# Performance work log

Hardware: AMD Instinct MI355X
Metric: run time of the kernel (lower is better)

## Reference

```python
import jax, jax.numpy as jnp
import numpy as np

NUM_EMBEDDINGS = 16384
EMBEDDING_DIM = 256
B, C, H, W = 8, 256, 32, 32


def _l2_normalize(x, axis=-1, eps=1e-12):
    # matches torch.nn.functional.normalize(p=2): x / max(||x||, eps)
    n = jnp.sqrt(jnp.sum(x * x, axis=axis, keepdims=True))
    return x / jnp.maximum(n, eps)


def setup_inputs() -> dict:
    key = jax.random.key(0)
    k1, k2 = jax.random.split(key)
    z = jax.random.normal(k1, (B, C, H, W), dtype=jnp.float32)
    embedding_weight = jax.random.normal(k2, (NUM_EMBEDDINGS, EMBEDDING_DIM), dtype=jnp.float32)
    return {"z": z, "embedding_weight": embedding_weight}


def reference(z, embedding_weight):
    batch_size, channels, height, width = z.shape
    # [B,C,H,W] -> [B,H,W,C] -> [N, D]
    z_flat = jnp.transpose(z, (0, 2, 3, 1)).reshape(-1, EMBEDDING_DIM)
    z_flat = _l2_normalize(z_flat)                 # l2_norm=True
    emb = _l2_normalize(embedding_weight)
    # squared distances: ||z||^2 + ||e||^2 - 2 z e^T  -> [N, K]
    d = (jnp.sum(z_flat * z_flat, axis=1, keepdims=True)
         + jnp.sum(emb * emb, axis=1)
         - 2.0 * jnp.matmul(z_flat, emb.T))
    indices = jnp.argmin(d, axis=1)                # [N]
    z_q = emb[indices].reshape(batch_size, height, width, EMBEDDING_DIM)
    z_q = jnp.transpose(z_q, (0, 3, 1, 2))         # [B,C,H,W]
    indices = indices.reshape(batch_size, height, width)
    return z_q, indices
```

## Files before the change

kernel.cpp:

```cpp
#include <hip/hip_runtime.h>

#define NUM_E   16384
#define DIM     256
#define NROWS   8192
#define HW      1024
#define BM      128
#define BN      128
#define BK      32
#define NCB     (NUM_E / BN)
#define GATE    2.5e-3f
#define TAUC    2.5e-3f
#define EHID    2.5e-3
#define MAXC    16

#define SWZ(r) ((((r) >> 1) ^ ((r) >> 3)) & 3)

typedef __bf16 bf16x8 __attribute__((ext_vector_type(8)));
typedef float  f32x4  __attribute__((ext_vector_type(4)));
typedef float  f32x16 __attribute__((ext_vector_type(16)));

__device__ __forceinline__ unsigned short f2bf(float x) {
    unsigned u = __float_as_uint(x);
    unsigned r = (u + 0x7fffu + ((u >> 16) & 1u)) >> 16;
    return (unsigned short)r;
}
__device__ __forceinline__ void async_copy16(const void* g, void* l) {
    __builtin_amdgcn_global_load_lds(
        (const __attribute__((address_space(1))) unsigned int*)g,
        (__attribute__((address_space(3))) unsigned int*)l, 16, 0, 0);
}
__device__ __forceinline__ int imax(int a, int b) { return a > b ? a : b; }
__device__ __forceinline__ int imin(int a, int b) { return a < b ? a : b; }

__global__ void k_prep_z(const float* __restrict__ z, unsigned short* __restrict__ Zh) {
    __shared__ float T[64 * 68];
    __shared__ float P[16][68];
    __shared__ __align__(16) float Tinv[64];
    int t = threadIdx.x;
    int n0 = blockIdx.x * 64;
    int b = n0 >> 10, hw0 = n0 & 1023;
    {
        int cg = t >> 4, h4 = (t & 15) * 4;
        float4 s4 = make_float4(0.f, 0.f, 0.f, 0.f);
        const float* pz = z + (size_t)(b * DIM + cg * 16) * HW + hw0 + h4;
        #pragma unroll
        for (int cc = 0; cc < 16; cc++) {
            float4 v = *(const float4*)(pz + (size_t)cc * HW);
            s4.x += v.x * v.x; s4.y += v.y * v.y; s4.z += v.z * v.z; s4.w += v.w * v.w;
        }
        *(float4*)&P[cg][h4] = s4;
    }
    __syncthreads();
    if (t < 64) {
        float s = 0.f;
        #pragma unroll
        for (int cg = 0; cg < 16; cg++) s += P[cg][t];
        Tinv[t] = 1.0f / fmaxf(sqrtf(s), 1e-12f);
    }
    __syncthreads();
    for (int c0 = 0; c0 < DIM; c0 += 64) {
        #pragma unroll
        for (int i = 0; i < 4; i++) {
            int f = t + 256 * i;
            int cc = f >> 4, n4 = (f & 15) * 4;
            float4 v  = *(const float4*)(z + (size_t)(b * DIM + c0 + cc) * HW + hw0 + n4);
            float4 iv = *(const float4*)&Tinv[n4];
            v.x *= iv.x; v.y *= iv.y; v.z *= iv.z; v.w *= iv.w;
            *(float4*)&T[cc * 68 + n4] = v;
        }
        __syncthreads();
        #pragma unroll
        for (int i = 0; i < 4; i++) {
            int f = t + 256 * i;
            int nn = f >> 4, c4 = (f & 15) * 4;
            ushort4 h;
            h.x = f2bf(T[(c4+0)*68 + nn]);
            h.y = f2bf(T[(c4+1)*68 + nn]);
            h.z = f2bf(T[(c4+2)*68 + nn]);
            h.w = f2bf(T[(c4+3)*68 + nn]);
            *(ushort4*)(Zh + (size_t)(n0 + nn) * DIM + c0 + c4) = h;
        }
        __syncthreads();
    }
}

__global__ void k_prep_e(const float* __restrict__ emb, float* __restrict__ inv_e,
                         double* __restrict__ se2, unsigned short* __restrict__ Eh,
                         int* __restrict__ cnt, int* __restrict__ cnt2) {
    if (blockIdx.x == 0 && threadIdx.x == 0) { *cnt = 0; *cnt2 = 0; }
    int wv = threadIdx.x >> 6, lane = threadIdx.x & 63;
    int k = blockIdx.x * 4 + wv;
    float4 v = *(const float4*)(emb + (size_t)k * DIM + lane * 4);
    double sq = (double)v.x*v.x + (double)v.y*v.y + (double)v.z*v.z + (double)v.w*v.w;
    for (int off = 32; off > 0; off >>= 1) sq += __shfl_down(sq, off);
    double tot = fmax(__shfl(sq, 0), 1e-24);
    if (lane == 0) { se2[k] = tot; inv_e[k] = 1.0f / fmaxf((float)sqrt(tot), 1e-12f); }
    float s = 1.0f / fmaxf((float)sqrt(tot), 1e-12f);
    ushort4 h;
    h.x = f2bf(v.x * s); h.y = f2bf(v.y * s); h.z = f2bf(v.z * s); h.w = f2bf(v.w * s);
    *(ushort4*)(Eh + (size_t)k * DIM + lane * 4) = h;
}

__launch_bounds__(256, 3)
__global__ void k_score(const unsigned short* __restrict__ Zh,
                        const unsigned short* __restrict__ Eh, int2* __restrict__ part) {
    __shared__ __align__(16) int smem[12288];
    unsigned short* lds = (unsigned short*)smem;
    int* kv = smem;
    const int t = threadIdx.x, l = t & 63, w = t >> 6;
    const int wm = w >> 1, wn = w & 1;
    const int m0 = blockIdx.x * BM;
    const int nb = blockIdx.y * BN;
    const int l31 = l & 31, lh = l >> 5;
    const int sr = l >> 2, sp = l & 3;

    const unsigned short* gA0 = Zh + (size_t)m0 * DIM;
    const unsigned short* gB0 = Eh + (size_t)nb * DIM;

    f32x16 acc[2][2];
    #pragma unroll
    for (int i = 0; i < 2; i++)
        #pragma unroll
        for (int j = 0; j < 2; j++) acc[i][j] = (f32x16)2.0f;

    auto stage = [&](int dbase, int kc) {
        #pragma unroll
        for (int h = 0; h < 2; h++) {
            int sub = w * 2 + h;
            int r = sub * 16 + sr;
            int c = sp ^ SWZ(r);
            async_copy16(gA0 + (size_t)r * DIM + kc + c * 8, &lds[dbase + sub * 512]);
        }
        #pragma unroll
        for (int h = 0; h < 2; h++) {
            int sub = w * 2 + h;
            int r = sub * 16 + sr;
            int c = sp ^ SWZ(r);
            async_copy16(gB0 + (size_t)r * DIM + kc + c * 8, &lds[dbase + 4096 + sub * 512]);
        }
    };

    stage(0, 0);
    stage(8192, BK);
    for (int kt = 0; kt < DIM / BK; kt++) {
        const int base = (kt % 3) * 8192;
        if (kt < DIM / BK - 1) asm volatile("s_waitcnt vmcnt(4)" ::: "memory");
        else                   asm volatile("s_waitcnt vmcnt(0)" ::: "memory");
        __builtin_amdgcn_s_barrier();
        asm volatile("" ::: "memory");
        bf16x8 ah[2][2], bh[2][2];
        #pragma unroll
        for (int s = 0; s < 2; s++) {
            int c = 2 * s + lh;
            #pragma unroll
            for (int i = 0; i < 2; i++) {
                int r = wm * 64 + i * 32 + l31;
                ah[s][i] = *(const bf16x8*)&lds[base + r * 32 + ((c ^ SWZ(r)) * 8)];
            }
            #pragma unroll
            for (int j = 0; j < 2; j++) {
                int r = wn * 64 + j * 32 + l31;
                bh[s][j] = *(const bf16x8*)&lds[base + 4096 + r * 32 + ((c ^ SWZ(r)) * 8)];
            }
        }
        if (kt + 2 < DIM / BK) stage(((kt + 2) % 3) * 8192, (kt + 2) * BK);
        __builtin_amdgcn_s_setprio(1);
        #pragma unroll
        for (int s = 0; s < 2; s++)
            #pragma unroll
            for (int i = 0; i < 2; i++)
                #pragma unroll
                for (int j = 0; j < 2; j++)
                    acc[i][j] = __builtin_amdgcn_mfma_f32_32x32x16_bf16(ah[s][i], bh[s][j], acc[i][j], 0, 0, 0);
        __builtin_amdgcn_s_setprio(0);
    }
    __syncthreads();

    const int cb0 = wn * 64 + l31;
    int KA1 = 0, KA2 = 0, KB1 = 0, KB2 = 0;
    const int rl = t >> 2, q = t & 3;
    #pragma unroll
    for (int i = 0; i < 2; i++) {
        #pragma unroll
        for (int reg = 0; reg < 16; reg++) {
            int k0 = (__float_as_int(acc[i][0][reg]) & 0xFFFFFF00) | cb0;
            int k1 = (__float_as_int(acc[i][1][reg]) & 0xFFFFFF00) | (cb0 + 32);
            int K1 = imax(k0, k1), K2 = imin(k0, k1);
            int rr = wm * 32 + (reg & 3) + 8 * (reg >> 2) + 4 * lh;
            int slot = wn * 32 + l31;
            *(int2*)&kv[(rr * 66 + slot) * 2] = make_int2(K1, K2);
        }
        __syncthreads();
        int S1 = 0, S2 = 0;
        const int2* pr = (const int2*)&kv[(rl * 66 + q * 16) * 2];
        #pragma unroll
        for (int u = 0; u < 16; u++) {
            int2 e = pr[u];
            S2 = imax(imax(S2, e.y), imin(S1, e.x));
            S1 = imax(S1, e.x);
        }
        __syncthreads();
        #pragma unroll
        for (int d2 = 1; d2 <= 2; d2 <<= 1) {
            int o1 = __shfl_down(S1, d2), o2 = __shfl_down(S2, d2);
            S2 = imax(imax(S2, o2), imin(S1, o1));
            S1 = imax(S1, o1);
        }
        if (i == 0) { KA1 = S1; KA2 = S2; } else { KB1 = S1; KB2 = S2; }
    }
    if ((t & 3) == 0) {
        int rowA = (rl >> 5) * 64 + (rl & 31);
        int rowB = rowA + 32;
        part[(size_t)blockIdx.y * NROWS + m0 + rowA] = make_int2(KA1, KA2);
        part[(size_t)blockIdx.y * NROWS + m0 + rowB] = make_int2(KB1, KB2);
    }
}

__global__ void k_final(const int2* __restrict__ part, int* __restrict__ idx_ws,
                        float* __restrict__ out_idx, int* __restrict__ flags,
                        int* __restrict__ cnt, int* __restrict__ cand,
                        int* __restrict__ ccnt, float* __restrict__ v2q) {
    __shared__ int rK1[8][33], rK2[8][33], rS[8][33];
    __shared__ int bK1[32], bK2[32];
    __shared__ int lcc[32];
    __shared__ int lcand[32][MAXC];
    __shared__ int sv2[8][33];
    const int nl = threadIdx.x & 31, sc = threadIdx.x >> 5;
    const int n = blockIdx.x * 32 + nl;
    if (threadIdx.x < 32) lcc[threadIdx.x] = 0;
    int K1 = 0, K2 = 0, S1 = 0;
    for (int s = sc * 16; s < sc * 16 + 16; s++) {
        int2 e = part[(size_t)s * NROWS + n];
        S1 = (e.x > K1) ? s : S1;
        int nK2 = imax(imin(K1, e.x), imax(K2, e.y));
        K1 = imax(K1, e.x);
        K2 = nK2;
    }
    rK1[sc][nl] = K1; rK2[sc][nl] = K2; rS[sc][nl] = S1;
    __syncthreads();
    if (threadIdx.x < 32) {
        int W1 = 0, W2 = 0, WS = 0;
        #pragma unroll
        for (int s2 = 0; s2 < 8; s2++) {
            int e1 = rK1[s2][threadIdx.x], e2 = rK2[s2][threadIdx.x];
            WS = (e1 > W1) ? rS[s2][threadIdx.x] : WS;
            int nW2 = imax(imin(W1, e1), imax(W2, e2));
            W1 = imax(W1, e1);
            W2 = nW2;
        }
        int nn = blockIdx.x * 32 + threadIdx.x;
        int J1 = WS * BN + (W1 & 0xFF);
        idx_ws[nn] = J1;
        out_idx[nn] = (float)J1;
        bK1[threadIdx.x] = W1;
        bK2[threadIdx.x] = W2;
    }
    __syncthreads();
    int kthr = __float_as_int(__int_as_float(bK1[nl] & 0xFFFFFF00) - TAUC);
    int lv2 = 0;
    for (int s = sc * 16; s < sc * 16 + 16; s++) {
        int2 e = part[(size_t)s * NROWS + n];
        if (e.x >= kthr) {
            int pos = atomicAdd(&lcc[nl], 2);
            if (pos < MAXC)     lcand[nl][pos]     = s * BN + (e.x & 0xFF);
            if (pos + 1 < MAXC) lcand[nl][pos + 1] = s * BN + (e.y & 0xFF);
            lv2 = imax(lv2, e.y);
        }
    }
    sv2[sc][nl] = lv2;
    __syncthreads();
    if (threadIdx.x < 32) {
        int nn = blockIdx.x * 32 + threadIdx.x;
        float v1 = __int_as_float(bK1[threadIdx.x] & 0xFFFFFF00) - 2.0f;
        float v2 = __int_as_float(bK2[threadIdx.x] & 0xFFFFFF00) - 2.0f;
        if (v1 - v2 < GATE) {
            int m = 0;
            #pragma unroll
            for (int s2 = 0; s2 < 8; s2++) m = imax(m, sv2[s2][threadIdx.x]);
            int p = atomicAdd(cnt, 1);
            flags[p] = nn;
            ccnt[nn] = lcc[threadIdx.x];
            v2q[nn] = __int_as_float(m & 0xFFFFFF00) - 2.0f;
            #pragma unroll
            for (int j = 0; j < MAXC; j++) cand[nn * MAXC + j] = lcand[threadIdx.x][j];
        }
    }
}

__launch_bounds__(256)
__global__ void k_rescan_cand(const int* __restrict__ flags, const int* __restrict__ cnt,
                              const int* __restrict__ cand, const int* __restrict__ ccnt,
                              const float* __restrict__ v2q,
                              const float* __restrict__ z, const float* __restrict__ emb,
                              const double* __restrict__ se2,
                              int* __restrict__ idx_ws, float* __restrict__ out_idx,
                              int* __restrict__ flags2, int* __restrict__ cnt2) {
    __shared__ double zs[DIM];
    __shared__ double wv[4];
    __shared__ int    wi[4];
    const int t = threadIdx.x, l = t & 63, w = t >> 6;
    const int F = *cnt;
    for (int f = blockIdx.x; f < F; f += gridDim.x) {
        int n = flags[f];
        int C = ccnt[n];
        int b = n >> 10, hw = n & 1023;
        __syncthreads();
        zs[t] = (double)z[(size_t)(b * DIM + t) * HW + hw];
        __syncthreads();
        double best = -2e18; int bi = 0x7fffffff;
        if (C <= MAXC) {
            double z0 = zs[l*4], z1 = zs[l*4+1], z2 = zs[l*4+2], z3 = zs[l*4+3];
            for (int cix = w; cix < C; cix += 4) {
                int k = cand[n * MAXC + cix];
                float4 ev = *(const float4*)(emb + (size_t)k * DIM + l * 4);
                double d = z0 * (double)ev.x + z1 * (double)ev.y
                         + z2 * (double)ev.z + z3 * (double)ev.w;
                #pragma unroll
                for (int o = 32; o > 0; o >>= 1) d += __shfl_down(d, o);
                if (l == 0) {
                    double qv = d / sqrt(se2[k]);
                    if (qv > best || (qv == best && k < bi)) { best = qv; bi = k; }
                }
            }
        }
        if (l == 0) { wv[w] = best; wi[w] = bi; }
        __syncthreads();
        if (t == 0) {
            if (C > MAXC) {
                int p = atomicAdd(cnt2, 1); flags2[p] = n;
            } else {
                double B = wv[0]; int BI = wi[0];
                #pragma unroll
                for (int x = 1; x < 4; x++)
                    if (wv[x] > B || (wv[x] == B && wi[x] < BI)) { B = wv[x]; BI = wi[x]; }
                if ((double)v2q[n] >= B - EHID) {
                    int p = atomicAdd(cnt2, 1); flags2[p] = n;
                } else {
                    idx_ws[n] = BI; out_idx[n] = (float)BI;
                }
            }
        }
    }
}

__launch_bounds__(256)
__global__ void k_fullscan_part(const int* __restrict__ flags2, const int* __restrict__ cnt2,
                                const float* __restrict__ z, const float* __restrict__ emb,
                                const double* __restrict__ se2, double2* __restrict__ partial) {
    __shared__ double zs[DIM];
    __shared__ double wv[4];
    __shared__ int    wi[4];
    const int t = threadIdx.x, l = t & 63, w = t >> 6;
    const int W = (*cnt2) * 64;
    for (int item = blockIdx.x; item < W; item += gridDim.x) {
        int f = item >> 6, split = item & 63;
        int n = flags2[f];
        int b = n >> 10, hw = n & 1023;
        __syncthreads();
        zs[t] = (double)z[(size_t)(b * DIM + t) * HW + hw];
        __syncthreads();
        double z0 = zs[l*4], z1 = zs[l*4+1], z2 = zs[l*4+2], z3 = zs[l*4+3];
        double best = -2e18; int bi = 0;
        int kbase = split * 256 + w * 64;
        for (int p = 0; p < 64; p++) {
            int k = kbase + p;
            float4 ev = *(const float4*)(emb + (size_t)k * DIM + l * 4);
            double d = z0 * (double)ev.x + z1 * (double)ev.y
                     + z2 * (double)ev.z + z3 * (double)ev.w;
            #pragma unroll
            for (int o = 32; o > 0; o >>= 1) d += __shfl_down(d, o);
            if (l == 0) {
                double qv = d / sqrt(se2[k]);
                if (qv > best) { best = qv; bi = k; }
            }
        }
        if (l == 0) { wv[w] = best; wi[w] = bi; }
        __syncthreads();
        if (t == 0) {
            double B = wv[0]; int BI = wi[0];
            #pragma unroll
            for (int x = 1; x < 4; x++)
                if (wv[x] > B || (wv[x] == B && wi[x] < BI)) { B = wv[x]; BI = wi[x]; }
            partial[item] = make_double2(B, (double)BI);
        }
        __syncthreads();
    }
}

__global__ void k_fullscan_merge(const int* __restrict__ flags2, const int* __restrict__ cnt2,
                                 const double2* __restrict__ partial,
                                 int* __restrict__ idx_ws, float* __restrict__ out_idx) {
    const int F = *cnt2;
    const int l = threadIdx.x & 63, w = threadIdx.x >> 6;
    for (int f = blockIdx.x * 4 + w; f < F; f += gridDim.x * 4) {
        double2 e = partial[(size_t)f * 64 + l];
        double v = e.x; int i = (int)e.y;
        #pragma unroll
        for (int o = 32; o > 0; o >>= 1) {
            double ov = __shfl_down(v, o);
            int    oi = __shfl_down(i, o);
            if (ov > v || (ov == v && oi < i)) { v = ov; i = oi; }
        }
        if (l == 0) { int n = flags2[f]; idx_ws[n] = i; out_idx[n] = (float)i; }
    }
}

__global__ void k_zq(const int* __restrict__ idx_ws, const float* __restrict__ emb,
                     const float* __restrict__ inv_e, float* __restrict__ zq) {
    int t = threadIdx.x;
    int n = blockIdx.x * 256 + t;
    int b = n >> 10, hw = n & 1023;
    int c0 = blockIdx.y * 32;
    int id = idx_ws[n];
    float s = inv_e[id];
    const float* er = emb + (size_t)id * DIM;
    #pragma unroll
    for (int cc = 0; cc < 32; cc += 4) {
        float4 a = *(const float4*)(er + c0 + cc);
        zq[(size_t)(b * DIM + c0 + cc + 0) * HW + hw] = a.x * s;
        zq[(size_t)(b * DIM + c0 + cc + 1) * HW + hw] = a.y * s;
        zq[(size_t)(b * DIM + c0 + cc + 2) * HW + hw] = a.z * s;
        zq[(size_t)(b * DIM + c0 + cc + 3) * HW + hw] = a.w * s;
    }
}

extern "C" void kernel_launch(void* const* d_in, const int* in_sizes, int n_in,
                              void* d_out, int out_size, void* d_ws, size_t ws_size,
                              hipStream_t stream) {
    const float* z   = (const float*)d_in[0];
    const float* emb = (const float*)d_in[1];

    unsigned short* Zh = (unsigned short*)d_ws;
    unsigned short* Eh = Zh + (size_t)NROWS * DIM;
    float*  inv_e = (float*)(Eh + (size_t)NUM_E * DIM);
    float*  zpart = inv_e + NUM_E;
    int*    idx_ws = (int*)(zpart + 16 * NROWS);
    double* se2   = (double*)(idx_ws + NROWS);
    int*    flags = (int*)(se2 + NUM_E);
    int*    flags2 = flags + NROWS;
    int*    cand  = flags2 + NROWS;
    int*    ccnt  = cand + NROWS * MAXC;
    float*  v2q   = (float*)(ccnt + NROWS);
    int*    cnt   = (int*)(v2q + NROWS);
    int*    cnt2  = cnt + 1;

    float* zq      = (float*)d_out;
    float* out_idx = zq + (size_t)NROWS * DIM;
    int2*    part    = (int2*)zq;
    double2* partial = (double2*)zq;

    k_prep_z <<<NROWS / 64, 256, 0, stream>>>(z, Zh);
    k_prep_e <<<NUM_E / 4, 256, 0, stream>>>(emb, inv_e, se2, Eh, cnt, cnt2);
    k_score  <<<dim3(NROWS / BM, NCB), 256, 0, stream>>>(Zh, Eh, part);
    k_final  <<<NROWS / 32, 256, 0, stream>>>(part, idx_ws, out_idx, flags, cnt,
                                              cand, ccnt, v2q);
    k_rescan_cand  <<<1024, 256, 0, stream>>>(flags, cnt, cand, ccnt, v2q, z, emb,
                                              se2, idx_ws, out_idx, flags2, cnt2);
    k_fullscan_part<<<2048, 256, 0, stream>>>(flags2, cnt2, z, emb, se2, partial);
    k_fullscan_merge<<<64, 256, 0, stream>>>(flags2, cnt2, partial, idx_ws, out_idx);
    k_zq     <<<dim3(NROWS / 256, 8), 256, 0, stream>>>(idx_ws, emb, inv_e, zq);
}
```

Before: 195.2 us.

## Rewrite score GEMM with direct global loads, wider N tile, swizzled grid; split z prep

The score kernel drops LDS staging and async copies. Each wave now loads its bf16 fragments straight from global memory into registers with a two-stage ping-pong. The N tile doubles to 256, so each wave holds 2x4 accumulators, and occupancy drops to 2 blocks per SM. Blocks are remapped through a swizzled 1D grid to improve L2 locality. The z-norm partial sums move into a merged pre-kernel alongside the embedding normalisation, and k_prep_z is split over channel blocks for more parallelism. The changes trade LDS reuse and bank-conflict-free reads for fewer barriers, at the risk of redundant global or L2 traffic and register pressure.

```diff
diff --git a/kernel.cpp b/kernel.cpp
--- a/kernel.cpp
+++ b/kernel.cpp
@@ -5,18 +5,14 @@
 #define NROWS   8192
 #define HW      1024
 #define BM      128
-#define BN      128
-#define BK      32
+#define BN      256
 #define NCB     (NUM_E / BN)
 #define GATE    2.5e-3f
 #define TAUC    2.5e-3f
 #define EHID    2.5e-3
 #define MAXC    16
 
-#define SWZ(r) ((((r) >> 1) ^ ((r) >> 3)) & 3)
-
 typedef __bf16 bf16x8 __attribute__((ext_vector_type(8)));
-typedef float  f32x4  __attribute__((ext_vector_type(4)));
 typedef float  f32x16 __attribute__((ext_vector_type(16)));
 
 __device__ __forceinline__ unsigned short f2bf(float x) {
@@ -24,168 +20,151 @@
     unsigned r = (u + 0x7fffu + ((u >> 16) & 1u)) >> 16;
     return (unsigned short)r;
 }
-__device__ __forceinline__ void async_copy16(const void* g, void* l) {
-    __builtin_amdgcn_global_load_lds(
-        (const __attribute__((address_space(1))) unsigned int*)g,
-        (__attribute__((address_space(3))) unsigned int*)l, 16, 0, 0);
-}
 __device__ __forceinline__ int imax(int a, int b) { return a > b ? a : b; }
 __device__ __forceinline__ int imin(int a, int b) { return a < b ? a : b; }
-
-__global__ void k_prep_z(const float* __restrict__ z, unsigned short* __restrict__ Zh) {
+__device__ __forceinline__ bf16x8 ld16(const unsigned short* p) {
+    return *(const bf16x8*)p;
+}
+
+__global__ void k_pre(const float* __restrict__ z, const float* __restrict__ emb,
+                      float* __restrict__ zpart, float* __restrict__ inv_e,
+                      double* __restrict__ se2, unsigned short* __restrict__ Eh,
+                      int* __restrict__ cnt, int* __restrict__ cnt2) {
+    int bid = blockIdx.x;
+    if (bid < NUM_E / 4) {
+        if (bid == 0 && threadIdx.x == 0) { *cnt = 0; *cnt2 = 0; }
+        int wv = threadIdx.x >> 6, lane = threadIdx.x & 63;
+        int k = bid * 4 + wv;
+        float4 v = *(const float4*)(emb + (size_t)k * DIM + lane * 4);
+        double sq = (double)v.x*v.x + (double)v.y*v.y + (double)v.z*v.z + (double)v.w*v.w;
+        for (int off = 32; off > 0; off >>= 1) sq += __shfl_down(sq, off);
+        double tot = fmax(__shfl(sq, 0), 1e-24);
+        if (lane == 0) { se2[k] = tot; inv_e[k] = 1.0f / fmaxf((float)sqrt(tot), 1e-12f); }
+        float s = 1.0f / fmaxf((float)sqrt(tot), 1e-12f);
+        ushort4 h;
+        h.x = f2bf(v.x * s); h.y = f2bf(v.y * s); h.z = f2bf(v.z * s); h.w = f2bf(v.w * s);
+        *(ushort4*)(Eh + (size_t)k * DIM + lane * 4) = h;
+    } else {
+        int ib = bid - NUM_E / 4;
+        int n = (ib & 31) * 256 + threadIdx.x;
+        int cb = ib >> 5;
+        int b = n >> 10, hw = n & 1023;
+        const float* p = z + (size_t)(b * DIM + cb * 16) * HW + hw;
+        float s = 0.f;
+        #pragma unroll
+        for (int c = 0; c < 16; c++) { float v = p[c * HW]; s += v * v; }
+        zpart[cb * NROWS + n] = s;
+    }
+}
+
+__global__ void k_prep_z(const float* __restrict__ z, const float* __restrict__ zpart,
+                         unsigned short* __restrict__ Zh) {
     __shared__ float T[64 * 68];
-    __shared__ float P[16][68];
     __shared__ __align__(16) float Tinv[64];
     int t = threadIdx.x;
-    int n0 = blockIdx.x * 64;
+    int n0 = blockIdx.x * 64, c0 = blockIdx.y * 64;
     int b = n0 >> 10, hw0 = n0 & 1023;
-    {
-        int cg = t >> 4, h4 = (t & 15) * 4;
-        float4 s4 = make_float4(0.f, 0.f, 0.f, 0.f);
-        const float* pz = z + (size_t)(b * DIM + cg * 16) * HW + hw0 + h4;
-        #pragma unroll
-        for (int cc = 0; cc < 16; cc++) {
-            float4 v = *(const float4*)(pz + (size_t)cc * HW);
-            s4.x += v.x * v.x; s4.y += v.y * v.y; s4.z += v.z * v.z; s4.w += v.w * v.w;
-        }
-        *(float4*)&P[cg][h4] = s4;
-    }
-    __syncthreads();
     if (t < 64) {
         float s = 0.f;
         #pragma unroll
-        for (int cg = 0; cg < 16; cg++) s += P[cg][t];
+        for (int cb = 0; cb < 16; cb++) s += zpart[cb * NROWS + n0 + t];
         Tinv[t] = 1.0f / fmaxf(sqrtf(s), 1e-12f);
     }
     __syncthreads();
-    for (int c0 = 0; c0 < DIM; c0 += 64) {
-        #pragma unroll
-        for (int i = 0; i < 4; i++) {
-            int f = t + 256 * i;
-            int cc = f >> 4, n4 = (f & 15) * 4;
-            float4 v  = *(const float4*)(z + (size_t)(b * DIM + c0 + cc) * HW + hw0 + n4);
-            float4 iv = *(const float4*)&Tinv[n4];
-            v.x *= iv.x; v.y *= iv.y; v.z *= iv.z; v.w *= iv.w;
-            *(float4*)&T[cc * 68 + n4] = v;
-        }
-        __syncthreads();
-        #pragma unroll
-        for (int i = 0; i < 4; i++) {
-            int f = t + 256 * i;
-            int nn = f >> 4, c4 = (f & 15) * 4;
-            ushort4 h;
-            h.x = f2bf(T[(c4+0)*68 + nn]);
-            h.y = f2bf(T[(c4+1)*68 + nn]);
-            h.z = f2bf(T[(c4+2)*68 + nn]);
-            h.w = f2bf(T[(c4+3)*68 + nn]);
-            *(ushort4*)(Zh + (size_t)(n0 + nn) * DIM + c0 + c4) = h;
-        }
-        __syncthreads();
-    }
-}
-
-__global__ void k_prep_e(const float* __restrict__ emb, float* __restrict__ inv_e,
-                         double* __restrict__ se2, unsigned short* __restrict__ Eh,
-                         int* __restrict__ cnt, int* __restrict__ cnt2) {
-    if (blockIdx.x == 0 && threadIdx.x == 0) { *cnt = 0; *cnt2 = 0; }
-    int wv = threadIdx.x >> 6, lane = threadIdx.x & 63;
-    int k = blockIdx.x * 4 + wv;
-    float4 v = *(const float4*)(emb + (size_t)k * DIM + lane * 4);
-    double sq = (double)v.x*v.x + (double)v.y*v.y + (double)v.z*v.z + (double)v.w*v.w;
-    for (int off = 32; off > 0; off >>= 1) sq += __shfl_down(sq, off);
-    double tot = fmax(__shfl(sq, 0), 1e-24);
-    if (lane == 0) { se2[k] = tot; inv_e[k] = 1.0f / fmaxf((float)sqrt(tot), 1e-12f); }
-    float s = 1.0f / fmaxf((float)sqrt(tot), 1e-12f);
-    ushort4 h;
-    h.x = f2bf(v.x * s); h.y = f2bf(v.y * s); h.z = f2bf(v.z * s); h.w = f2bf(v.w * s);
-    *(ushort4*)(Eh + (size_t)k * DIM + lane * 4) = h;
-}
-
-__launch_bounds__(256, 3)
+    #pragma unroll
+    for (int i = 0; i < 4; i++) {
+        int f = t + 256 * i;
+        int cc = f >> 4, n4 = (f & 15) * 4;
+        float4 v  = *(const float4*)(z + (size_t)(b * DIM + c0 + cc) * HW + hw0 + n4);
+        float4 iv = *(const float4*)&Tinv[n4];
+        v.x *= iv.x; v.y *= iv.y; v.z *= iv.z; v.w *= iv.w;
+        *(float4*)&T[cc * 68 + n4] = v;
+    }
+    __syncthreads();
+    #pragma unroll
+    for (int i = 0; i < 4; i++) {
+        int f = t + 256 * i;
+        int nn = f >> 4, c4 = (f & 15) * 4;
+        ushort4 h;
+        h.x = f2bf(T[(c4+0)*68 + nn]);
+        h.y = f2bf(T[(c4+1)*68 + nn]);
+        h.z = f2bf(T[(c4+2)*68 + nn]);
+        h.w = f2bf(T[(c4+3)*68 + nn]);
+        *(ushort4*)(Zh + (size_t)(n0 + nn) * DIM + c0 + c4) = h;
+    }
+}
+
+__launch_bounds__(256, 2)
 __global__ void k_score(const unsigned short* __restrict__ Zh,
                         const unsigned short* __restrict__ Eh, int2* __restrict__ part) {
-    __shared__ __align__(16) int smem[12288];
-    unsigned short* lds = (unsigned short*)smem;
-    int* kv = smem;
+    __shared__ __align__(16) int kv[8448];
     const int t = threadIdx.x, l = t & 63, w = t >> 6;
     const int wm = w >> 1, wn = w & 1;
-    const int m0 = blockIdx.x * BM;
-    const int nb = blockIdx.y * BN;
+    int bid = blockIdx.x;
+    int rr2 = (bid & 7) * 512 + (bid >> 3);
+    int st = rr2 >> 6, wi = rr2 & 63;
+    const int m0 = ((st >> 3) * 8 + (wi >> 3)) * BM;
+    const int nb = ((st & 7) * 8 + (wi & 7)) * BN;
     const int l31 = l & 31, lh = l >> 5;
-    const int sr = l >> 2, sp = l & 3;
-
-    const unsigned short* gA0 = Zh + (size_t)m0 * DIM;
-    const unsigned short* gB0 = Eh + (size_t)nb * DIM;
-
-    f32x16 acc[2][2];
+
+    const unsigned short* pa0 = Zh + (size_t)(m0 + wm * 64 + l31) * DIM + lh * 8;
+    const unsigned short* pa1 = pa0 + 32 * DIM;
+    const unsigned short* pb0 = Eh + (size_t)(nb + wn * 128 + l31) * DIM + lh * 8;
+    const unsigned short* pb1 = pb0 + 32 * DIM;
+    const unsigned short* pb2 = pb0 + 64 * DIM;
+    const unsigned short* pb3 = pb0 + 96 * DIM;
+
+    f32x16 acc[2][4];
     #pragma unroll
     for (int i = 0; i < 2; i++)
         #pragma unroll
-        for (int j = 0; j < 2; j++) acc[i][j] = (f32x16)2.0f;
-
-    auto stage = [&](int dbase, int kc) {
-        #pragma unroll
-        for (int h = 0; h < 2; h++) {
-            int sub = w * 2 + h;
-            int r = sub * 16 + sr;
-            int c = sp ^ SWZ(r);
-            async_copy16(gA0 + (size_t)r * DIM + kc + c * 8, &lds[dbase + sub * 512]);
-        }
-        #pragma unroll
-        for (int h = 0; h < 2; h++) {
-            int sub = w * 2 + h;
-            int r = sub * 16 + sr;
-            int c = sp ^ SWZ(r);
-            async_copy16(gB0 + (size_t)r * DIM + kc + c * 8, &lds[dbase + 4096 + sub * 512]);
-        }
-    };
-
-    stage(0, 0);
-    stage(8192, BK);
-    for (int kt = 0; kt < DIM / BK; kt++) {
-        const int base = (kt % 3) * 8192;
-        if (kt < DIM / BK - 1) asm volatile("s_waitcnt vmcnt(4)" ::: "memory");
-        else                   asm volatile("s_waitcnt vmcnt(0)" ::: "memory");
-        __builtin_amdgcn_s_barrier();
-        asm volatile("" ::: "memory");
-        bf16x8 ah[2][2], bh[2][2];
-        #pragma unroll
-        for (int s = 0; s < 2; s++) {
-            int c = 2 * s + lh;
-            #pragma unroll
-            for (int i = 0; i < 2; i++) {
-                int r = wm * 64 + i * 32 + l31;
-                ah[s][i] = *(const bf16x8*)&lds[base + r * 32 + ((c ^ SWZ(r)) * 8)];
-            }
-            #pragma unroll
-            for (int j = 0; j < 2; j++) {
-                int r = wn * 64 + j * 32 + l31;
-                bh[s][j] = *(const bf16x8*)&lds[base + 4096 + r * 32 + ((c ^ SWZ(r)) * 8)];
-            }
-        }
-        if (kt + 2 < DIM / BK) stage(((kt + 2) % 3) * 8192, (kt + 2) * BK);
-        __builtin_amdgcn_s_setprio(1);
-        #pragma unroll
-        for (int s = 0; s < 2; s++)
-            #pragma unroll
-            for (int i = 0; i < 2; i++)
-                #pragma unroll
-                for (int j = 0; j < 2; j++)
-                    acc[i][j] = __builtin_amdgcn_mfma_f32_32x32x16_bf16(ah[s][i], bh[s][j], acc[i][j], 0, 0, 0);
-        __builtin_amdgcn_s_setprio(0);
-    }
-    __syncthreads();
-
-    const int cb0 = wn * 64 + l31;
+        for (int j = 0; j < 4; j++) acc[i][j] = (f32x16)2.0f;
+
+    bf16x8 Pa0, Pa1, Pb0, Pb1, Pb2, Pb3;
+    bf16x8 Qa0, Qa1, Qb0, Qb1, Qb2, Qb3;
+
+#define LDSET(PR, OFF) \
+    PR##a0 = ld16(pa0 + (OFF)); PR##a1 = ld16(pa1 + (OFF)); \
+    PR##b0 = ld16(pb0 + (OFF)); PR##b1 = ld16(pb1 + (OFF)); \
+    PR##b2 = ld16(pb2 + (OFF)); PR##b3 = ld16(pb3 + (OFF));
+#define MFSET(PR) \
+    __builtin_amdgcn_s_setprio(1); \
+    acc[0][0] = __builtin_amdgcn_mfma_f32_32x32x16_bf16(PR##a0, PR##b0, acc[0][0], 0, 0, 0); \
+    acc[0][1] = __builtin_amdgcn_mfma_f32_32x32x16_bf16(PR##a0, PR##b1, acc[0][1], 0, 0, 0); \
+    acc[0][2] = __builtin_amdgcn_mfma_f32_32x32x16_bf16(PR##a0, PR##b2, acc[0][2], 0, 0, 0); \
+    acc[0][3] = __builtin_amdgcn_mfma_f32_32x32x16_bf16(PR##a0, PR##b3, acc[0][3], 0, 0, 0); \
+    acc[1][0] = __builtin_amdgcn_mfma_f32_32x32x16_bf16(PR##a1, PR##b0, acc[1][0], 0, 0, 0); \
+    acc[1][1] = __builtin_amdgcn_mfma_f32_32x32x16_bf16(PR##a1, PR##b1, acc[1][1], 0, 0, 0); \
+    acc[1][2] = __builtin_amdgcn_mfma_f32_32x32x16_bf16(PR##a1, PR##b2, acc[1][2], 0, 0, 0); \
+    acc[1][3] = __builtin_amdgcn_mfma_f32_32x32x16_bf16(PR##a1, PR##b3, acc[1][3], 0, 0, 0); \
+    __builtin_amdgcn_s_setprio(0);
+
+    LDSET(P, 0);
+    #pragma unroll
+    for (int h = 0; h < 8; h++) {
+        LDSET(Q, (2 * h + 1) * 16);
+        MFSET(P);
+        if (h < 7) { LDSET(P, (2 * h + 2) * 16); }
+        MFSET(Q);
+    }
+#undef LDSET
+#undef MFSET
+
+    const int colbase = wn * 128 + l31;
     int KA1 = 0, KA2 = 0, KB1 = 0, KB2 = 0;
     const int rl = t >> 2, q = t & 3;
     #pragma unroll
     for (int i = 0; i < 2; i++) {
         #pragma unroll
         for (int reg = 0; reg < 16; reg++) {
-            int k0 = (__float_as_int(acc[i][0][reg]) & 0xFFFFFF00) | cb0;
-            int k1 = (__float_as_int(acc[i][1][reg]) & 0xFFFFFF00) | (cb0 + 32);
-            int K1 = imax(k0, k1), K2 = imin(k0, k1);
+            int k0 = (__float_as_int(acc[i][0][reg]) & 0xFFFFFF00) | colbase;
+            int k1 = (__float_as_int(acc[i][1][reg]) & 0xFFFFFF00) | (colbase + 32);
+            int k2 = (__float_as_int(acc[i][2][reg]) & 0xFFFFFF00) | (colbase + 64);
+            int k3 = (__float_as_int(acc[i][3][reg]) & 0xFFFFFF00) | (colbase + 96);
+            int a = imax(k0, k1), b = imin(k0, k1);
+            int c = imax(k2, k3), d = imin(k2, k3);
+            int K1 = imax(a, c);
+            int K2 = imax(imin(a, c), imax(b, d));
             int rr = wm * 32 + (reg & 3) + 8 * (reg >> 2) + 4 * lh;
             int slot = wn * 32 + l31;
             *(int2*)&kv[(rr * 66 + slot) * 2] = make_int2(K1, K2);
@@ -211,8 +190,9 @@
     if ((t & 3) == 0) {
         int rowA = (rl >> 5) * 64 + (rl & 31);
         int rowB = rowA + 32;
-        part[(size_t)blockIdx.y * NROWS + m0 + rowA] = make_int2(KA1, KA2);
-        part[(size_t)blockIdx.y * NROWS + m0 + rowB] = make_int2(KB1, KB2);
+        int seg = nb / BN;
+        part[(size_t)seg * NROWS + m0 + rowA] = make_int2(KA1, KA2);
+        part[(size_t)seg * NROWS + m0 + rowB] = make_int2(KB1, KB2);
     }
 }
 
@@ -229,7 +209,7 @@
     const int n = blockIdx.x * 32 + nl;
     if (threadIdx.x < 32) lcc[threadIdx.x] = 0;
     int K1 = 0, K2 = 0, S1 = 0;
-    for (int s = sc * 16; s < sc * 16 + 16; s++) {
+    for (int s = sc * 8; s < sc * 8 + 8; s++) {
         int2 e = part[(size_t)s * NROWS + n];
         S1 = (e.x > K1) ? s : S1;
         int nK2 = imax(imin(K1, e.x), imax(K2, e.y));
@@ -258,7 +238,7 @@
     __syncthreads();
     int kthr = __float_as_int(__int_as_float(bK1[nl] & 0xFFFFFF00) - TAUC);
     int lv2 = 0;
-    for (int s = sc * 16; s < sc * 16 + 16; s++) {
+    for (int s = sc * 8; s < sc * 8 + 8; s++) {
         int2 e = part[(size_t)s * NROWS + n];
         if (e.x >= kthr) {
             int pos = atomicAdd(&lcc[nl], 2);
@@ -449,9 +429,9 @@
     int2*    part    = (int2*)zq;
     double2* partial = (double2*)zq;
 
-    k_prep_z <<<NROWS / 64, 256, 0, stream>>>(z, Zh);
-    k_prep_e <<<NUM_E / 4, 256, 0, stream>>>(emb, inv_e, se2, Eh, cnt, cnt2);
-    k_score  <<<dim3(NROWS / BM, NCB), 256, 0, stream>>>(Zh, Eh, part);
+    k_pre    <<<NUM_E / 4 + 512, 256, 0, stream>>>(z, emb, zpart, inv_e, se2, Eh, cnt, cnt2);
+    k_prep_z <<<dim3(NROWS / 64, DIM / 64), 256, 0, stream>>>(z, zpart, Zh);
+    k_score  <<<(NROWS / BM) * NCB, 256, 0, stream>>>(Zh, Eh, part);
     k_final  <<<NROWS / 32, 256, 0, stream>>>(part, idx_ws, out_idx, flags, cnt,
                                               cand, ccnt, v2q);
     k_rescan_cand  <<<1024, 256, 0, stream>>>(flags, cnt, cand, ccnt, v2q, z, emb,
```

Measured after the change: 279.7 us. 43.3% more time.
